# Kernel tuning notes

Hardware: AMD Instinct MI355X
Metric: run time of the kernel (lower is better)

## Reference

```python
import jax, jax.numpy as jnp
import numpy as np

C = 256
C8 = C // 8
B, D, H, W = 2, 16, 64, 64


def setup_inputs() -> dict:
    key = jax.random.key(0)
    ks = jax.random.split(key, 8)
    s = 0.05
    return {
        "x1": jax.random.normal(ks[0], (B, C, D, H, W), dtype=jnp.float32),
        "x2": jax.random.normal(ks[1], (B, C, D, H, W), dtype=jnp.float32),
        "Wq": jax.random.normal(ks[2], (C8, C), dtype=jnp.float32) * s,
        "bq": jax.random.normal(ks[3], (C8,), dtype=jnp.float32) * s,
        "Wk": jax.random.normal(ks[4], (C8, C), dtype=jnp.float32) * s,
        "bk": jax.random.normal(ks[5], (C8,), dtype=jnp.float32) * s,
        "Wv": jax.random.normal(ks[6], (C, C), dtype=jnp.float32) * s,
        "bv": jax.random.normal(ks[7], (C,), dtype=jnp.float32) * s,
    }


def _conv1x1(x, Wt, b):
    # 1x1x1 Conv3d == channel-mixing linear: x [B,Cin,D,H,W], Wt [Cout,Cin]
    return jnp.einsum('bcdhw,oc->bodhw', x, Wt) + b[None, :, None, None, None]


def reference(x1, x2, Wq, bq, Wk, bk, Wv, bv):
    q = _conv1x1(x1, Wq, bq)   # [B,C8,D,H,W]
    k = _conv1x1(x2, Wk, bk)   # [B,C8,D,H,W]
    v = _conv1x1(x2, Wv, bv)   # [B,C, D,H,W]
    # Non-softmax bilinear attention over the W axis, batched over (b,d,h)
    attn = jnp.einsum('bcdhx,bcdhy->bdhxy', q, k)        # [B,D,H,W,W]
    out = jnp.einsum('bdhxy,bcdhy->bcdhx', attn, v)      # [B,C,D,H,W]
    return out
```

## Files before the change

kernel.cpp:

```cpp
#include <hip/hip_runtime.h>

#define NB   2
#define ND   16
#define NH   64
#define DHW  65536
#define HW   4096
#define CDHW 16777216

typedef __attribute__((ext_vector_type(4))) float f32x4;
typedef __attribute__((ext_vector_type(8))) short bf16x8;
typedef unsigned short ushort_t;

#define MFMA16(a, b, c) __builtin_amdgcn_mfma_f32_16x16x32_bf16((a), (b), (c), 0, 0, 0)

#define WS_WQH 0
#define WS_WQL 8192
#define WS_WKH 16384
#define WS_WKL 24576
#define WS_WVH 32768
#define WS_WVL 98304
#define WS_WEIGHT_USHORTS 163840
#define WS_AH  (WS_WEIGHT_USHORTS)
#define WS_AL  (WS_AH + 8388608)
#define WS_FULL_BYTES ((size_t)(WS_WEIGHT_USHORTS + 16777216) * 2)

__device__ __forceinline__ void split_val(float f, short& h, short& l) {
  unsigned int u = __builtin_bit_cast(unsigned int, f);
  h = (short)(unsigned short)(u >> 16);
  float fh = __builtin_bit_cast(float, u & 0xffff0000u);
  float r = f - fh;
  l = (short)(unsigned short)(__builtin_bit_cast(unsigned int, r) >> 16);
}

__device__ __forceinline__ void load_split8(const float* __restrict__ p, bf16x8& h8, bf16x8& l8) {
  float4 a = *(const float4*)p;
  float4 b = *(const float4*)(p + 4);
  float f[8] = {a.x, a.y, a.z, a.w, b.x, b.y, b.z, b.w};
#pragma unroll
  for (int j = 0; j < 8; ++j) {
    short hh, ll;
    split_val(f[j], hh, ll);
    h8[j] = hh; l8[j] = ll;
  }
}

__device__ __forceinline__ int swzb(int row, int colb) {
  return row * 128 + (((colb) & ~15) ^ ((row & 7) << 4)) + ((colb) & 15);
}

__global__ void prep_w(const float* __restrict__ Wq, const float* __restrict__ Wk,
                       const float* __restrict__ Wv, ushort_t* __restrict__ ws) {
  int idx = blockIdx.x * 256 + threadIdx.x;
  const float* src; int off; ushort_t *H, *L;
  if (idx < 8192)       { src = Wq; off = idx;         H = ws + WS_WQH; L = ws + WS_WQL; }
  else if (idx < 16384) { src = Wk; off = idx - 8192;  H = ws + WS_WKH; L = ws + WS_WKL; }
  else if (idx < 81920) { src = Wv; off = idx - 16384; H = ws + WS_WVH; L = ws + WS_WVL; }
  else return;
  short h, l;
  split_val(src[off], h, l);
  H[off] = (ushort_t)h;
  L[off] = (ushort_t)l;
}

__global__ __launch_bounds__(256, 2) void qk_kernel(
    const float* __restrict__ x1, const float* __restrict__ x2,
    const float* __restrict__ bq, const float* __restrict__ bk,
    ushort_t* __restrict__ ws)
{
  __shared__ char qsmem[32768];
  const int tid  = threadIdx.x;
  const int lane = tid & 63;
  const int wv   = tid >> 6;
  const int l15  = lane & 15;
  const int g    = lane >> 4;

  const int grp = blockIdx.x * 4 + wv;
  const int b   = grp >> 10;
  const int rem = grp & 1023;
  const int d   = rem >> 6;
  const int h   = rem & 63;
  const size_t base = (size_t)b * CDHW + (size_t)d * HW + (size_t)h * 64;
  const float* x1p = x1 + base;
  const float* x2p = x2 + base;

  float* buf = (float*)(qsmem + wv * 8192);

  const ushort_t* WqH = ws + WS_WQH;
  const ushort_t* WqL = ws + WS_WQL;
  const ushort_t* WkH = ws + WS_WKH;
  const ushort_t* WkL = ws + WS_WKL;

  f32x4 qacc[2][4], kacc[2][4];
#pragma unroll
  for (int mt = 0; mt < 2; ++mt) {
    int r0 = mt * 16 + 4 * g;
    f32x4 bqv = (f32x4){bq[r0], bq[r0 + 1], bq[r0 + 2], bq[r0 + 3]};
    f32x4 bkv = (f32x4){bk[r0], bk[r0 + 1], bk[r0 + 2], bk[r0 + 3]};
#pragma unroll
    for (int nt = 0; nt < 4; ++nt) { qacc[mt][nt] = bqv; kacc[mt][nt] = bkv; }
  }

  const int rrow = (lane >> 4);
  const int rcol = (lane & 15) * 4;

  float4 rfA[8], rfB[8];
  auto loadc = [&](float4* rf, int i) {
    const float* src = (i < 8 ? x1p : x2p) + (size_t)(32 * (i & 7)) * DHW;
#pragma unroll
    for (int k = 0; k < 8; ++k)
      rf[k] = *(const float4*)(src + (size_t)(4 * k + rrow) * DHW + rcol);
  };
  auto writec = [&](const float4* rf) {
#pragma unroll
    for (int k = 0; k < 8; ++k)
      *(float4*)&buf[(4 * k + rrow) * 64 + rcol] = rf[k];
  };
  auto compute = [&](int i, f32x4 (&acc)[2][4], const ushort_t* Wh, const ushort_t* Wl) {
    const int kg0 = 32 * (i & 7) + 8 * g;
    bf16x8 bh[4], bl[4];
#pragma unroll
    for (int nt = 0; nt < 4; ++nt) {
#pragma unroll
      for (int j = 0; j < 8; ++j) {
        float f = buf[(8 * g + j) * 64 + nt * 16 + l15];
        short hh, ll;
        split_val(f, hh, ll);
        bh[nt][j] = hh; bl[nt][j] = ll;
      }
    }
#pragma unroll
    for (int mt = 0; mt < 2; ++mt) {
      bf16x8 wh = *(const bf16x8*)&Wh[(size_t)(mt * 16 + l15) * 256 + kg0];
      bf16x8 wl = *(const bf16x8*)&Wl[(size_t)(mt * 16 + l15) * 256 + kg0];
#pragma unroll
      for (int nt = 0; nt < 4; ++nt) {
        acc[mt][nt] = MFMA16(wh, bh[nt], acc[mt][nt]);
        acc[mt][nt] = MFMA16(wh, bl[nt], acc[mt][nt]);
        acc[mt][nt] = MFMA16(wl, bh[nt], acc[mt][nt]);
      }
    }
  };

  loadc(rfA, 0);
#pragma unroll
  for (int i2 = 0; i2 < 8; ++i2) {
    const int i0 = 2 * i2, i1 = 2 * i2 + 1;
    loadc(rfB, i1);
    writec(rfA);
    if (i0 < 8) compute(i0, qacc, WqH, WqL); else compute(i0, kacc, WkH, WkL);
    if (i1 + 1 < 16) loadc(rfA, i1 + 1);
    writec(rfB);
    if (i1 < 8) compute(i1, qacc, WqH, WqL); else compute(i1, kacc, WkH, WkL);
  }

  ushort_t* ex = (ushort_t*)buf;
#pragma unroll
  for (int mt = 0; mt < 2; ++mt)
#pragma unroll
    for (int nt = 0; nt < 4; ++nt)
#pragma unroll
      for (int r = 0; r < 4; ++r) {
        short hh, ll;
        split_val(qacc[mt][nt][r], hh, ll);
        int x = nt * 16 + l15;
        ex[x * 32 + mt * 16 + 4 * g + r]        = (ushort_t)hh;
        ex[2048 + x * 32 + mt * 16 + 4 * g + r] = (ushort_t)ll;
      }
  bf16x8 qh8[4], ql8[4];
#pragma unroll
  for (int mt = 0; mt < 4; ++mt) {
    qh8[mt] = *(const bf16x8*)&ex[(mt * 16 + l15) * 32 + 8 * g];
    ql8[mt] = *(const bf16x8*)&ex[2048 + (mt * 16 + l15) * 32 + 8 * g];
  }
#pragma unroll
  for (int mt = 0; mt < 2; ++mt)
#pragma unroll
    for (int nt = 0; nt < 4; ++nt)
#pragma unroll
      for (int r = 0; r < 4; ++r) {
        short hh, ll;
        split_val(kacc[mt][nt][r], hh, ll);
        int y = nt * 16 + l15;
        ex[y * 32 + mt * 16 + 4 * g + r]        = (ushort_t)hh;
        ex[2048 + y * 32 + mt * 16 + 4 * g + r] = (ushort_t)ll;
      }
  bf16x8 kh8[4], kl8[4];
#pragma unroll
  for (int nt = 0; nt < 4; ++nt) {
    kh8[nt] = *(const bf16x8*)&ex[(nt * 16 + l15) * 32 + 8 * g];
    kl8[nt] = *(const bf16x8*)&ex[2048 + (nt * 16 + l15) * 32 + 8 * g];
  }
  f32x4 aacc[4][4];
#pragma unroll
  for (int mt = 0; mt < 4; ++mt)
#pragma unroll
    for (int nt = 0; nt < 4; ++nt) {
      f32x4 a = (f32x4){0.f, 0.f, 0.f, 0.f};
      a = MFMA16(qh8[mt], kh8[nt], a);
      a = MFMA16(qh8[mt], kl8[nt], a);
      a = MFMA16(ql8[mt], kh8[nt], a);
      aacc[mt][nt] = a;
    }
  ushort_t* Ah = ws + WS_AH + (size_t)grp * 4096;
  ushort_t* Al = ws + WS_AL + (size_t)grp * 4096;
#pragma unroll
  for (int mt = 0; mt < 4; ++mt)
#pragma unroll
    for (int nt = 0; nt < 4; ++nt)
#pragma unroll
      for (int r = 0; r < 4; ++r) {
        short hh, ll;
        split_val(aacc[mt][nt][r], hh, ll);
        int x = mt * 16 + 4 * g + r, y = nt * 16 + l15;
        Ah[x * 64 + y] = (ushort_t)hh;
        Al[x * 64 + y] = (ushort_t)ll;
      }
}

#define B_OFF_XTH  0
#define B_OFF_XTL  8192
#define B_OFF_XLIN 16384
#define B_SMEM     32768

__global__ __launch_bounds__(256, 4) void xattn_v2(
    const float* __restrict__ x2, const float* __restrict__ bv,
    const ushort_t* __restrict__ wsp, float* __restrict__ out)
{
  __shared__ char smem[B_SMEM];
  char*  XthB = smem + B_OFF_XTH;
  char*  XtlB = smem + B_OFF_XTL;
  float* Xlin = (float*)(smem + B_OFF_XLIN);

  const int tid  = threadIdx.x;
  const int lane = tid & 63;
  const int wv   = tid >> 6;
  const int l15  = lane & 15;
  const int g    = lane >> 4;

  const int bid   = blockIdx.x;
  const int grp   = bid >> 1;
  const int chalf = bid & 1;
  const int cbase = chalf * 128;
  const int b   = grp >> 10;
  const int rem = grp & 1023;
  const int d   = rem >> 6;
  const int h   = rem & 63;
  const size_t base = (size_t)b * CDHW + (size_t)d * HW + (size_t)h * 64;
  const float* x2p = x2 + base;

  const ushort_t* WvH = wsp + WS_WVH;
  const ushort_t* WvL = wsp + WS_WVL;
  const ushort_t* AhW = wsp + WS_AH + (size_t)grp * 4096;
  const ushort_t* AlW = wsp + WS_AL + (size_t)grp * 4096;

  float4 pf[4];
  auto issue_pf = [&](const float* __restrict__ src) {
#pragma unroll
    for (int i = 0; i < 4; ++i) {
      int ch = 16 * wv + g + 4 * i;
      pf[i] = *(const float4*)(src + (size_t)ch * DHW + 4 * l15);
    }
  };
  auto write_xlin = [&]() {
#pragma unroll
    for (int i = 0; i < 4; ++i) {
      int ch = 16 * wv + g + 4 * i;
      *(float4*)&Xlin[ch * 64 + 4 * l15] = pf[i];
    }
  };
  auto passB = [&]() {
#pragma unroll
    for (int bb = 0; bb < 2; ++bb) {
      int c0 = 16 * wv + 8 * bb;
      bf16x8 h8, l8;
#pragma unroll
      for (int j = 0; j < 8; ++j) {
        float f = Xlin[(c0 + j) * 64 + lane];
        short hh, ll;
        split_val(f, hh, ll);
        h8[j] = hh; l8[j] = ll;
      }
      *(bf16x8*)(XthB + swzb(lane, c0 * 2)) = h8;
      *(bf16x8*)(XtlB + swzb(lane, c0 * 2)) = l8;
    }
  };
  auto ldsx = [&](const char* B, int row, int ko) -> bf16x8 {
    return *(const bf16x8*)(B + swzb(row, ko * 2));
  };

  f32x4 vacc[2][4];
#pragma unroll
  for (int mt = 0; mt < 2; ++mt) {
    int r0 = cbase + 32 * wv + mt * 16 + 4 * g;
    f32x4 bb = (f32x4){bv[r0], bv[r0 + 1], bv[r0 + 2], bv[r0 + 3]};
#pragma unroll
    for (int nt = 0; nt < 4; ++nt) vacc[mt][nt] = bb;
  }

  issue_pf(x2p);
  write_xlin();
  __syncthreads();

  for (int t = 0; t < 4; ++t) {
    passB();
    __syncthreads();
    if (t < 3) issue_pf(x2p + (size_t)(t + 1) * 64 * DHW);
#pragma unroll
    for (int ks = 0; ks < 2; ++ks) {
      const int ko = ks * 32 + 8 * g;
      const int kg = t * 64 + ko;
      bf16x8 xh[4], xl[4];
#pragma unroll
      for (int nt = 0; nt < 4; ++nt) {
        xh[nt] = ldsx(XthB, nt * 16 + l15, ko);
        xl[nt] = ldsx(XtlB, nt * 16 + l15, ko);
      }
      __builtin_amdgcn_s_setprio(1);
#pragma unroll
      for (int mt = 0; mt < 2; ++mt) {
        bf16x8 wh = *(const bf16x8*)&WvH[(size_t)(cbase + 32 * wv + mt * 16 + l15) * 256 + kg];
        bf16x8 wl = *(const bf16x8*)&WvL[(size_t)(cbase + 32 * wv + mt * 16 + l15) * 256 + kg];
#pragma unroll
        for (int nt = 0; nt < 4; ++nt) {
          vacc[mt][nt] = MFMA16(wh, xh[nt], vacc[mt][nt]);
          vacc[mt][nt] = MFMA16(wh, xl[nt], vacc[mt][nt]);
          vacc[mt][nt] = MFMA16(wl, xh[nt], vacc[mt][nt]);
        }
      }
      __builtin_amdgcn_s_setprio(0);
    }
    if (t < 3) write_xlin();
    __syncthreads();
  }

  {
    char* VhB = smem + B_OFF_XLIN + wv * 4096;
    char* VlB = VhB + 2048;
#pragma unroll
    for (int mt = 0; mt < 2; ++mt) {
#pragma unroll
      for (int nt = 0; nt < 4; ++nt)
#pragma unroll
        for (int r = 0; r < 4; ++r) {
          short hh, ll;
          split_val(vacc[mt][nt][r], hh, ll);
          int colb = (nt * 16 + l15) * 2;
          *(ushort_t*)(VhB + swzb(4 * g + r, colb)) = (ushort_t)hh;
          *(ushort_t*)(VlB + swzb(4 * g + r, colb)) = (ushort_t)ll;
        }
      f32x4 oacc[4];
#pragma unroll
      for (int nt = 0; nt < 4; ++nt) oacc[nt] = (f32x4){0.f, 0.f, 0.f, 0.f};
      __builtin_amdgcn_s_setprio(1);
#pragma unroll
      for (int ys = 0; ys < 2; ++ys) {
        const int yo = ys * 32 + 8 * g;
        bf16x8 vh8 = *(const bf16x8*)(VhB + swzb(l15, yo * 2));
        bf16x8 vl8 = *(const bf16x8*)(VlB + swzb(l15, yo * 2));
#pragma unroll
        for (int nt = 0; nt < 4; ++nt) {
          bf16x8 ah8 = *(const bf16x8*)&AhW[(nt * 16 + l15) * 64 + yo];
          bf16x8 al8 = *(const bf16x8*)&AlW[(nt * 16 + l15) * 64 + yo];
          oacc[nt] = MFMA16(vh8, ah8, oacc[nt]);
          oacc[nt] = MFMA16(vh8, al8, oacc[nt]);
          oacc[nt] = MFMA16(vl8, ah8, oacc[nt]);
        }
      }
      __builtin_amdgcn_s_setprio(0);
#pragma unroll
      for (int nt = 0; nt < 4; ++nt)
#pragma unroll
        for (int r = 0; r < 4; ++r)
          out[base + (size_t)(cbase + 32 * wv + mt * 16 + 4 * g + r) * DHW + nt * 16 + l15] = oacc[nt][r];
    }
  }
}

#define XT_LD 72
#define QK_LD 40
#define A_LD  72
#define VB_LD 72
#define F_OFF_XTH 0
#define F_OFF_XTL 9216
#define F_OFF_R2  18432
#define F_OFF_KH  18432
#define F_OFF_KL  23552
#define F_OFF_AH  0
#define F_OFF_AL  9216
#define F_OFF_QH  36864
#define F_OFF_QL  41984
#define F_SMEM 47104

__global__ __launch_bounds__(256, 3) void xattn_fallback(
    const float* __restrict__ x1, const float* __restrict__ x2,
    const float* __restrict__ Wq, const float* __restrict__ bq,
    const float* __restrict__ Wk, const float* __restrict__ bk,
    const float* __restrict__ Wv, const float* __restrict__ bv,
    float* __restrict__ out)
{
  __shared__ char smem[F_SMEM];
  ushort_t* Xth  = (ushort_t*)(smem + F_OFF_XTH);
  ushort_t* Xtl  = (ushort_t*)(smem + F_OFF_XTL);
  float*    Xlin = (float*)(smem + F_OFF_R2);
  ushort_t* Kh   = (ushort_t*)(smem + F_OFF_KH);
  ushort_t* Kl   = (ushort_t*)(smem + F_OFF_KL);
  ushort_t* Vb   = (ushort_t*)(smem + F_OFF_R2);
  ushort_t* Ah   = (ushort_t*)(smem + F_OFF_AH);
  ushort_t* Al   = (ushort_t*)(smem + F_OFF_AL);
  ushort_t* Qh   = (ushort_t*)(smem + F_OFF_QH);
  ushort_t* Ql   = (ushort_t*)(smem + F_OFF_QL);

  const int tid  = threadIdx.x;
  const int lane = tid & 63;
  const int wv   = tid >> 6;
  const int l15  = lane & 15;
  const int g    = lane >> 4;

  const int grp = blockIdx.x;
  const int b   = grp >> 10;
  const int rem = grp & 1023;
  const int d   = rem >> 6;
  const int h   = rem & 63;
  const size_t base = (size_t)b * CDHW + (size_t)d * HW + (size_t)h * 64;

  auto passA = [&](const float* __restrict__ src) {
#pragma unroll
    for (int i = 0; i < 4; ++i) {
      int ch = 16 * wv + (lane >> 4) + 4 * i;
      int c4 = (lane & 15) << 2;
      float4 v = *(const float4*)(src + (size_t)ch * DHW + c4);
      *(float4*)&Xlin[ch * 66 + c4] = v;
    }
  };
  auto passB = [&]() {
#pragma unroll
    for (int bb = 0; bb < 2; ++bb) {
      int c0 = 16 * wv + 8 * bb;
      bf16x8 h8, l8;
#pragma unroll
      for (int j = 0; j < 8; ++j) {
        float f = Xlin[(c0 + j) * 66 + lane];
        short hh, ll;
        split_val(f, hh, ll);
        h8[j] = hh; l8[j] = ll;
      }
      *(bf16x8*)&Xth[lane * XT_LD + c0] = h8;
      *(bf16x8*)&Xtl[lane * XT_LD + c0] = l8;
    }
  };

  {
    f32x4 qacc[2];
#pragma unroll
    for (int mt = 0; mt < 2; ++mt) {
      int r0 = mt * 16 + 4 * g;
      qacc[mt] = (f32x4){bq[r0], bq[r0 + 1], bq[r0 + 2], bq[r0 + 3]};
    }
    const float* x1p = x1 + base;
    for (int t = 0; t < 4; ++t) {
      passA(x1p + (size_t)t * 64 * DHW);
      __syncthreads();
      passB();
      __syncthreads();
#pragma unroll
      for (int ks = 0; ks < 2; ++ks) {
        const int ko = ks * 32 + 8 * g;
        const int kg = t * 64 + ko;
        bf16x8 bh = *(const bf16x8*)&Xth[(16 * wv + l15) * XT_LD + ko];
        bf16x8 bl = *(const bf16x8*)&Xtl[(16 * wv + l15) * XT_LD + ko];
#pragma unroll
        for (int mt = 0; mt < 2; ++mt) {
          bf16x8 wh, wl;
          load_split8(Wq + (size_t)(mt * 16 + l15) * 256 + kg, wh, wl);
          qacc[mt] = MFMA16(wh, bh, qacc[mt]);
          qacc[mt] = MFMA16(wh, bl, qacc[mt]);
          qacc[mt] = MFMA16(wl, bh, qacc[mt]);
        }
      }
      __syncthreads();
    }
    const int x = 16 * wv + l15;
#pragma unroll
    for (int mt = 0; mt < 2; ++mt)
#pragma unroll
      for (int r = 0; r < 4; ++r) {
        short hh, ll;
        split_val(qacc[mt][r], hh, ll);
        Qh[x * QK_LD + mt * 16 + 4 * g + r] = (ushort_t)hh;
        Ql[x * QK_LD + mt * 16 + 4 * g + r] = (ushort_t)ll;
      }
  }

  f32x4 vacc[4][4];
  {
    f32x4 kacc[2];
#pragma unroll
    for (int mt = 0; mt < 2; ++mt) {
      int r0 = mt * 16 + 4 * g;
      kacc[mt] = (f32x4){bk[r0], bk[r0 + 1], bk[r0 + 2], bk[r0 + 3]};
    }
#pragma unroll
    for (int mt = 0; mt < 4; ++mt) {
      int r0 = 64 * wv + mt * 16 + 4 * g;
      f32x4 bb = (f32x4){bv[r0], bv[r0 + 1], bv[r0 + 2], bv[r0 + 3]};
#pragma unroll
      for (int nt = 0; nt < 4; ++nt) vacc[mt][nt] = bb;
    }
    const float* x2p = x2 + base;
    for (int t = 0; t < 4; ++t) {
      passA(x2p + (size_t)t * 64 * DHW);
      __syncthreads();
      passB();
      __syncthreads();
#pragma unroll
      for (int ks = 0; ks < 2; ++ks) {
        const int ko = ks * 32 + 8 * g;
        const int kg = t * 64 + ko;
        bf16x8 xh[4], xl[4];
#pragma unroll
        for (int nt = 0; nt < 4; ++nt) {
          xh[nt] = *(const bf16x8*)&Xth[(nt * 16 + l15) * XT_LD + ko];
          xl[nt] = *(const bf16x8*)&Xtl[(nt * 16 + l15) * XT_LD + ko];
        }
        {
          bf16x8 bh = *(const bf16x8*)&Xth[(16 * wv + l15) * XT_LD + ko];
          bf16x8 bl = *(const bf16x8*)&Xtl[(16 * wv + l15) * XT_LD + ko];
#pragma unroll
          for (int mt = 0; mt < 2; ++mt) {
            bf16x8 wh, wl;
            load_split8(Wk + (size_t)(mt * 16 + l15) * 256 + kg, wh, wl);
            kacc[mt] = MFMA16(wh, bh, kacc[mt]);
            kacc[mt] = MFMA16(wh, bl, kacc[mt]);
            kacc[mt] = MFMA16(wl, bh, kacc[mt]);
          }
        }
#pragma unroll
        for (int mt = 0; mt < 4; ++mt) {
          bf16x8 wh, wl;
          load_split8(Wv + (size_t)(64 * wv + mt * 16 + l15) * 256 + kg, wh, wl);
#pragma unroll
          for (int nt = 0; nt < 4; ++nt) {
            vacc[mt][nt] = MFMA16(wh, xh[nt], vacc[mt][nt]);
            vacc[mt][nt] = MFMA16(wh, xl[nt], vacc[mt][nt]);
            vacc[mt][nt] = MFMA16(wl, xh[nt], vacc[mt][nt]);
          }
        }
      }
      __syncthreads();
    }
    const int y = 16 * wv + l15;
#pragma unroll
    for (int mt = 0; mt < 2; ++mt)
#pragma unroll
      for (int r = 0; r < 4; ++r) {
        short hh, ll;
        split_val(kacc[mt][r], hh, ll);
        Kh[y * QK_LD + mt * 16 + 4 * g + r] = (ushort_t)hh;
        Kl[y * QK_LD + mt * 16 + 4 * g + r] = (ushort_t)ll;
      }
  }
  __syncthreads();

  {
    const int y = 16 * wv + l15;
    bf16x8 kh = *(const bf16x8*)&Kh[y * QK_LD + 8 * g];
    bf16x8 kl = *(const bf16x8*)&Kl[y * QK_LD + 8 * g];
    f32x4 acc[4];
#pragma unroll
    for (int mt = 0; mt < 4; ++mt) acc[mt] = (f32x4){0.f, 0.f, 0.f, 0.f};
#pragma unroll
    for (int mt = 0; mt < 4; ++mt) {
      bf16x8 qh = *(const bf16x8*)&Qh[(mt * 16 + l15) * QK_LD + 8 * g];
      bf16x8 ql = *(const bf16x8*)&Ql[(mt * 16 + l15) * QK_LD + 8 * g];
      acc[mt] = MFMA16(qh, kh, acc[mt]);
      acc[mt] = MFMA16(qh, kl, acc[mt]);
      acc[mt] = MFMA16(ql, kh, acc[mt]);
    }
#pragma unroll
    for (int mt = 0; mt < 4; ++mt)
#pragma unroll
      for (int r = 0; r < 4; ++r) {
        short hh, ll;
        split_val(acc[mt][r], hh, ll);
        Ah[(mt * 16 + 4 * g + r) * A_LD + y] = (ushort_t)hh;
        Al[(mt * 16 + 4 * g + r) * A_LD + y] = (ushort_t)ll;
      }
  }
  __syncthreads();

  {
    ushort_t* Vh = Vb + wv * 2304;
    ushort_t* Vl = Vh + 1152;
    const int cb = 64 * wv;
#pragma unroll
    for (int mt = 0; mt < 4; ++mt) {
#pragma unroll
      for (int nt = 0; nt < 4; ++nt)
#pragma unroll
        for (int r = 0; r < 4; ++r) {
          short hh, ll;
          split_val(vacc[mt][nt][r], hh, ll);
          Vh[(4 * g + r) * VB_LD + nt * 16 + l15] = (ushort_t)hh;
          Vl[(4 * g + r) * VB_LD + nt * 16 + l15] = (ushort_t)ll;
        }
      f32x4 oacc[4];
#pragma unroll
      for (int nt = 0; nt < 4; ++nt) oacc[nt] = (f32x4){0.f, 0.f, 0.f, 0.f};
#pragma unroll
      for (int ys = 0; ys < 2; ++ys) {
        const int yo = ys * 32 + 8 * g;
        bf16x8 vh8 = *(const bf16x8*)&Vh[l15 * VB_LD + yo];
        bf16x8 vl8 = *(const bf16x8*)&Vl[l15 * VB_LD + yo];
#pragma unroll
        for (int nt = 0; nt < 4; ++nt) {
          bf16x8 ah8 = *(const bf16x8*)&Ah[(nt * 16 + l15) * A_LD + yo];
          bf16x8 al8 = *(const bf16x8*)&Al[(nt * 16 + l15) * A_LD + yo];
          oacc[nt] = MFMA16(vh8, ah8, oacc[nt]);
          oacc[nt] = MFMA16(vh8, al8, oacc[nt]);
          oacc[nt] = MFMA16(vl8, ah8, oacc[nt]);
        }
      }
#pragma unroll
      for (int nt = 0; nt < 4; ++nt)
#pragma unroll
        for (int r = 0; r < 4; ++r)
          out[base + (size_t)(cb + mt * 16 + 4 * g + r) * DHW + nt * 16 + l15] = oacc[nt][r];
    }
  }
}

extern "C" void kernel_launch(void* const* d_in, const int* in_sizes, int n_in,
                              void* d_out, int out_size, void* d_ws, size_t ws_size,
                              hipStream_t stream)
{
  const float* x1 = (const float*)d_in[0];
  const float* x2 = (const float*)d_in[1];
  const float* Wq = (const float*)d_in[2];
  const float* bq = (const float*)d_in[3];
  const float* Wk = (const float*)d_in[4];
  const float* bk = (const float*)d_in[5];
  const float* Wv = (const float*)d_in[6];
  const float* bv = (const float*)d_in[7];
  float* out = (float*)d_out;

  if (d_ws && ws_size >= WS_FULL_BYTES) {
    ushort_t* ws = (ushort_t*)d_ws;
    hipLaunchKernelGGL(prep_w, dim3(320), dim3(256), 0, stream, Wq, Wk, Wv, ws);
    hipLaunchKernelGGL(qk_kernel, dim3(512), dim3(256), 0, stream, x1, x2, bq, bk, ws);
    hipLaunchKernelGGL(xattn_v2, dim3(4096), dim3(256), 0, stream, x2, bv, ws, out);
  } else {
    hipLaunchKernelGGL(xattn_fallback, dim3(NB * ND * NH), dim3(256), 0, stream,
                       x1, x2, Wq, bq, Wk, bk, Wv, bv, out);
  }
}
```

Before: 245.1 us.

## Stage attention matrix in LDS and hoist weight loads ahead of passB

The attention kernel now copies the per-row A hi/lo matrices from global memory into swizzled LDS once per block. The final V·A products then read them from LDS instead of global. The Wv weight fragments for each t-step are loaded before the passB transpose and barrier, so their global latency overlaps that work. The qk kernel loads both weight tiles up front. Shared memory grows from 32KB to 48KB and launch bounds drop from 4 to 3 blocks per SM, which lowers occupancy and raises register pressure.

```diff
diff --git a/kernel.cpp b/kernel.cpp
--- a/kernel.cpp
+++ b/kernel.cpp
@@ -117,6 +117,10 @@
   };
   auto compute = [&](int i, f32x4 (&acc)[2][4], const ushort_t* Wh, const ushort_t* Wl) {
     const int kg0 = 32 * (i & 7) + 8 * g;
+    bf16x8 wh0 = *(const bf16x8*)&Wh[(size_t)(l15) * 256 + kg0];
+    bf16x8 wl0 = *(const bf16x8*)&Wl[(size_t)(l15) * 256 + kg0];
+    bf16x8 wh1 = *(const bf16x8*)&Wh[(size_t)(16 + l15) * 256 + kg0];
+    bf16x8 wl1 = *(const bf16x8*)&Wl[(size_t)(16 + l15) * 256 + kg0];
     bf16x8 bh[4], bl[4];
 #pragma unroll
     for (int nt = 0; nt < 4; ++nt) {
@@ -129,15 +133,13 @@
       }
     }
 #pragma unroll
-    for (int mt = 0; mt < 2; ++mt) {
-      bf16x8 wh = *(const bf16x8*)&Wh[(size_t)(mt * 16 + l15) * 256 + kg0];
-      bf16x8 wl = *(const bf16x8*)&Wl[(size_t)(mt * 16 + l15) * 256 + kg0];
-#pragma unroll
-      for (int nt = 0; nt < 4; ++nt) {
-        acc[mt][nt] = MFMA16(wh, bh[nt], acc[mt][nt]);
-        acc[mt][nt] = MFMA16(wh, bl[nt], acc[mt][nt]);
-        acc[mt][nt] = MFMA16(wl, bh[nt], acc[mt][nt]);
-      }
+    for (int nt = 0; nt < 4; ++nt) {
+      acc[0][nt] = MFMA16(wh0, bh[nt], acc[0][nt]);
+      acc[0][nt] = MFMA16(wh0, bl[nt], acc[0][nt]);
+      acc[0][nt] = MFMA16(wl0, bh[nt], acc[0][nt]);
+      acc[1][nt] = MFMA16(wh1, bh[nt], acc[1][nt]);
+      acc[1][nt] = MFMA16(wh1, bl[nt], acc[1][nt]);
+      acc[1][nt] = MFMA16(wl1, bh[nt], acc[1][nt]);
     }
   };
 
@@ -219,16 +221,20 @@
 
 #define B_OFF_XTH  0
 #define B_OFF_XTL  8192
-#define B_OFF_XLIN 16384
-#define B_SMEM     32768
-
-__global__ __launch_bounds__(256, 4) void xattn_v2(
+#define B_OFF_AH   16384
+#define B_OFF_AL   24576
+#define B_OFF_XLIN 32768
+#define B_SMEM     49152
+
+__global__ __launch_bounds__(256, 3) void xattn_v3(
     const float* __restrict__ x2, const float* __restrict__ bv,
     const ushort_t* __restrict__ wsp, float* __restrict__ out)
 {
   __shared__ char smem[B_SMEM];
   char*  XthB = smem + B_OFF_XTH;
   char*  XtlB = smem + B_OFF_XTL;
+  char*  AhL  = smem + B_OFF_AH;
+  char*  AlL  = smem + B_OFF_AL;
   float* Xlin = (float*)(smem + B_OFF_XLIN);
 
   const int tid  = threadIdx.x;
@@ -298,17 +304,38 @@
   }
 
   issue_pf(x2p);
+  {
+#pragma unroll
+    for (int rr = 0; rr < 2; ++rr) {
+      int idx = tid + rr * 256;
+      int row = idx >> 3;
+      int seg = idx & 7;
+      bf16x8 vh = *(const bf16x8*)&AhW[row * 64 + seg * 8];
+      bf16x8 vl = *(const bf16x8*)&AlW[row * 64 + seg * 8];
+      *(bf16x8*)(AhL + swzb(row, seg * 16)) = vh;
+      *(bf16x8*)(AlL + swzb(row, seg * 16)) = vl;
+    }
+  }
   write_xlin();
   __syncthreads();
 
   for (int t = 0; t < 4; ++t) {
+    bf16x8 w_h[2][2], w_l[2][2];
+#pragma unroll
+    for (int ks = 0; ks < 2; ++ks) {
+      const int kg = t * 64 + ks * 32 + 8 * g;
+#pragma unroll
+      for (int mt = 0; mt < 2; ++mt) {
+        w_h[ks][mt] = *(const bf16x8*)&WvH[(size_t)(cbase + 32 * wv + mt * 16 + l15) * 256 + kg];
+        w_l[ks][mt] = *(const bf16x8*)&WvL[(size_t)(cbase + 32 * wv + mt * 16 + l15) * 256 + kg];
+      }
+    }
     passB();
     __syncthreads();
     if (t < 3) issue_pf(x2p + (size_t)(t + 1) * 64 * DHW);
 #pragma unroll
     for (int ks = 0; ks < 2; ++ks) {
       const int ko = ks * 32 + 8 * g;
-      const int kg = t * 64 + ko;
       bf16x8 xh[4], xl[4];
 #pragma unroll
       for (int nt = 0; nt < 4; ++nt) {
@@ -318,13 +345,11 @@
       __builtin_amdgcn_s_setprio(1);
 #pragma unroll
       for (int mt = 0; mt < 2; ++mt) {
-        bf16x8 wh = *(const bf16x8*)&WvH[(size_t)(cbase + 32 * wv + mt * 16 + l15) * 256 + kg];
-        bf16x8 wl = *(const bf16x8*)&WvL[(size_t)(cbase + 32 * wv + mt * 16 + l15) * 256 + kg];
 #pragma unroll
         for (int nt = 0; nt < 4; ++nt) {
-          vacc[mt][nt] = MFMA16(wh, xh[nt], vacc[mt][nt]);
-          vacc[mt][nt] = MFMA16(wh, xl[nt], vacc[mt][nt]);
-          vacc[mt][nt] = MFMA16(wl, xh[nt], vacc[mt][nt]);
+          vacc[mt][nt] = MFMA16(w_h[ks][mt], xh[nt], vacc[mt][nt]);
+          vacc[mt][nt] = MFMA16(w_h[ks][mt], xl[nt], vacc[mt][nt]);
+          vacc[mt][nt] = MFMA16(w_l[ks][mt], xh[nt], vacc[mt][nt]);
         }
       }
       __builtin_amdgcn_s_setprio(0);
@@ -359,8 +384,8 @@
         bf16x8 vl8 = *(const bf16x8*)(VlB + swzb(l15, yo * 2));
 #pragma unroll
         for (int nt = 0; nt < 4; ++nt) {
-          bf16x8 ah8 = *(const bf16x8*)&AhW[(nt * 16 + l15) * 64 + yo];
-          bf16x8 al8 = *(const bf16x8*)&AlW[(nt * 16 + l15) * 64 + yo];
+          bf16x8 ah8 = ldsx(AhL, nt * 16 + l15, yo);
+          bf16x8 al8 = ldsx(AlL, nt * 16 + l15, yo);
           oacc[nt] = MFMA16(vh8, ah8, oacc[nt]);
           oacc[nt] = MFMA16(vh8, al8, oacc[nt]);
           oacc[nt] = MFMA16(vl8, ah8, oacc[nt]);
@@ -647,7 +672,7 @@
     ushort_t* ws = (ushort_t*)d_ws;
     hipLaunchKernelGGL(prep_w, dim3(320), dim3(256), 0, stream, Wq, Wk, Wv, ws);
     hipLaunchKernelGGL(qk_kernel, dim3(512), dim3(256), 0, stream, x1, x2, bq, bk, ws);
-    hipLaunchKernelGGL(xattn_v2, dim3(4096), dim3(256), 0, stream, x2, bv, ws, out);
+    hipLaunchKernelGGL(xattn_v3, dim3(4096), dim3(256), 0, stream, x2, bv, ws, out);
   } else {
     hipLaunchKernelGGL(xattn_fallback, dim3(NB * ND * NH), dim3(256), 0, stream,
                        x1, x2, Wq, bq, Wk, bk, Wv, bv, out);
```

New measurement: 214.4 us. 12.5% less time.
